# Optimization experiments

Measured on AMD Instinct MI355X. Metric: run time of the kernel, lower is better.

The kernel has to match this reference:

```python
import jax, jax.numpy as jnp
import numpy as np

B, T, C = 2, 1536, 1536
H, K, V = 8, 64, 192
NPF = 192            # num_position_features
NB = NPF // 6        # basis per class for central_mask, asymmetric (6 components)
FD = 2 * NB          # actual positional feature dim after sign concat
R = 2 * T - 1


def central_mask_feats(positions, num_basis, seq_length):
    # widths grow geometrically so only |pos| < width activates (central mask)
    pow_rate = np.exp(np.log(seq_length + 1) / num_basis).astype(np.float32)
    widths = jnp.power(pow_rate, jnp.arange(1, num_basis + 1, dtype=jnp.float32)) - 1.0
    return (widths[None, :] > jnp.abs(positions)[:, None]).astype(jnp.float32)


def position_features(positions, seq_length):
    emb = central_mask_feats(positions, NB, seq_length)                 # [R, NB]
    return jnp.concatenate([emb, jnp.sign(positions)[:, None] * emb], axis=-1)  # [R, 2*NB]


def relative_shift(x):
    # x: [B, H, T, 2T-1] -> [B, H, T, T] (Transformer-XL shift trick)
    b, h, t, r = x.shape
    x = jnp.pad(x, ((0, 0), (0, 0), (0, 0), (1, 0)))    # [B,H,T,2T]
    x = x.reshape(b, h, 2 * t, t)[:, :, 1:, :]          # [B,H,2T-1,T]
    x = x.reshape(b, h, t, 2 * t - 1)[..., :t]          # [B,H,T,T]
    return x


def setup_inputs() -> dict:
    key = jax.random.key(0)
    ks = jax.random.split(key, 9)
    s = 0.02
    return {
        "x": jax.random.normal(ks[0], (B, T, C), jnp.float32),
        "Wq": jax.random.normal(ks[1], (C, H * K), jnp.float32) * s,
        "Wk": jax.random.normal(ks[2], (C, H * K), jnp.float32) * s,
        "Wv": jax.random.normal(ks[3], (C, H * V), jnp.float32) * s,
        "Wrk": jax.random.normal(ks[4], (FD, H * K), jnp.float32) * s,
        "r_w_bias": jax.random.normal(ks[5], (1, H, 1, K), jnp.float32) * s,
        "r_r_bias": jax.random.normal(ks[6], (1, H, 1, K), jnp.float32) * s,
        "Wo": jax.random.normal(ks[7], (H * V, H * V), jnp.float32) * s,
        "bo": jnp.zeros((H * V,), jnp.float32),
    }


def reference(x, Wq, Wk, Wv, Wrk, r_w_bias, r_r_bias, Wo, bo):
    b, t, _ = x.shape
    q = (x @ Wq).reshape(b, t, H, K).transpose(0, 2, 1, 3)   # [B,H,T,K]
    k = (x @ Wk).reshape(b, t, H, K).transpose(0, 2, 1, 3)
    v = (x @ Wv).reshape(b, t, H, V).transpose(0, 2, 1, 3)   # [B,H,T,V]
    q = q * (K ** -0.5)                                       # scaling=True

    # content logits with content bias r_w_bias
    content = jnp.einsum('bhqd,bhkd->bhqk', q + r_w_bias, k)  # [B,H,T,T]

    # relative position logits with position bias r_r_bias
    dists = jnp.arange(-(t - 1), t, dtype=jnp.float32)        # [2T-1]
    pos = position_features(dists, t)                         # [2T-1, FD]
    r_k = (pos @ Wrk).reshape(R, H, K).transpose(1, 0, 2)     # [H,2T-1,K]
    rel = jnp.einsum('bhqd,hrd->bhqr', q + r_r_bias, r_k)     # [B,H,T,2T-1]
    rel = relative_shift(rel)                                 # [B,H,T,T]

    logits = content + rel                                    # content_position_bias=True
    w = jax.nn.softmax(logits, axis=-1)
    out = jnp.einsum('bhqk,bhkv->bhqv', w, v)                 # [B,H,T,V]
    out = out.transpose(0, 2, 1, 3).reshape(b, t, H * V)      # [B,T,H*V]
    return out @ Wo + bo
```

## Files before the change

kernel.cpp:

```cpp
#include <hip/hip_runtime.h>
#include <hip/hip_bf16.h>
#include <math.h>

#define T_SEQ 1536
#define CDIM  1536
#define HEADS 8
#define DK    64
#define DV    192
#define HK    (HEADS * DK)
#define HV    (HEADS * DV)
#define RWIN  (2 * T_SEQ - 1)

typedef __attribute__((ext_vector_type(8))) short bf16x8;
typedef __attribute__((ext_vector_type(4))) float f32x4;

__device__ __forceinline__ unsigned short f2bf(float v) {
  __hip_bfloat16 h = __float2bfloat16(v);
  return *reinterpret_cast<unsigned short*>(&h);
}
__device__ __forceinline__ float bf2f(unsigned short u) {
  unsigned int x = ((unsigned int)u) << 16;
  union { unsigned int i; float f; } c; c.i = x; return c.f;
}

__global__ __launch_bounds__(256) void cast_bf16_kernel(
    const float* __restrict__ in, unsigned short* __restrict__ out, int n)
{
  const int i = (blockIdx.x * 256 + threadIdx.x) * 4;
  if (i >= n) return;
  const float4 v = *reinterpret_cast<const float4*>(&in[i]);
  ushort4 o;
  o.x = f2bf(v.x); o.y = f2bf(v.y); o.z = f2bf(v.z); o.w = f2bf(v.w);
  *reinterpret_cast<ushort4*>(&out[i]) = o;
}

__global__ __launch_bounds__(256) void tcast_kernel(
    const float* __restrict__ W, unsigned short* __restrict__ Wt, int Kd, int N)
{
  __shared__ float tile[32][33];
  const int n0 = blockIdx.x * 32, k0 = blockIdx.y * 32;
  const int tx = threadIdx.x, ty = threadIdx.y;
  #pragma unroll
  for (int i = 0; i < 32; i += 8)
    tile[ty + i][tx] = W[(size_t)(k0 + ty + i) * N + n0 + tx];
  __syncthreads();
  #pragma unroll
  for (int i = 0; i < 32; i += 8)
    Wt[(size_t)(n0 + ty + i) * Kd + k0 + tx] = f2bf(tile[tx][ty + i]);
}

template<int OMODE>
__global__ __launch_bounds__(256) void gemm_bf16_kernel(
    const unsigned short* __restrict__ A, const unsigned short* __restrict__ Bt,
    void* __restrict__ Cp, int M, int N, int Kd, float scale,
    const float* __restrict__ bias)
{
  constexpr int LDK = 40;
  __shared__ unsigned short As[128 * LDK];
  __shared__ unsigned short Bs[128 * LDK];
  const int tid = threadIdx.x;
  const int lane = tid & 63, wave = tid >> 6;
  const int wr = wave >> 1, wc = wave & 1;
  const int m0 = blockIdx.x * 128, n0 = blockIdx.y * 128;

  const int lr = tid >> 2;
  const int lc = (tid & 3) * 8;
  const int frow = lane & 15;
  const int fk = (lane >> 4) * 8;

  f32x4 acc[4][4];
  #pragma unroll
  for (int i = 0; i < 4; ++i)
    #pragma unroll
    for (int j = 0; j < 4; ++j) acc[i][j] = (f32x4){0.f, 0.f, 0.f, 0.f};

  uint4 a0 = *reinterpret_cast<const uint4*>(&A[(size_t)(m0 + lr) * Kd + lc]);
  uint4 a1 = *reinterpret_cast<const uint4*>(&A[(size_t)(m0 + 64 + lr) * Kd + lc]);
  uint4 b0 = *reinterpret_cast<const uint4*>(&Bt[(size_t)(n0 + lr) * Kd + lc]);
  uint4 b1 = *reinterpret_cast<const uint4*>(&Bt[(size_t)(n0 + 64 + lr) * Kd + lc]);

  for (int k0 = 0; k0 < Kd; k0 += 32) {
    __syncthreads();
    *reinterpret_cast<uint4*>(&As[lr * LDK + lc]) = a0;
    *reinterpret_cast<uint4*>(&As[(64 + lr) * LDK + lc]) = a1;
    *reinterpret_cast<uint4*>(&Bs[lr * LDK + lc]) = b0;
    *reinterpret_cast<uint4*>(&Bs[(64 + lr) * LDK + lc]) = b1;
    __syncthreads();
    if (k0 + 32 < Kd) {
      const int kn = k0 + 32;
      a0 = *reinterpret_cast<const uint4*>(&A[(size_t)(m0 + lr) * Kd + kn + lc]);
      a1 = *reinterpret_cast<const uint4*>(&A[(size_t)(m0 + 64 + lr) * Kd + kn + lc]);
      b0 = *reinterpret_cast<const uint4*>(&Bt[(size_t)(n0 + lr) * Kd + kn + lc]);
      b1 = *reinterpret_cast<const uint4*>(&Bt[(size_t)(n0 + 64 + lr) * Kd + kn + lc]);
    }
    bf16x8 af[4], bfr[4];
    #pragma unroll
    for (int mi = 0; mi < 4; ++mi)
      af[mi] = *reinterpret_cast<const bf16x8*>(&As[(wr * 64 + mi * 16 + frow) * LDK + fk]);
    #pragma unroll
    for (int ni = 0; ni < 4; ++ni)
      bfr[ni] = *reinterpret_cast<const bf16x8*>(&Bs[(wc * 64 + ni * 16 + frow) * LDK + fk]);
    #pragma unroll
    for (int mi = 0; mi < 4; ++mi)
      #pragma unroll
      for (int ni = 0; ni < 4; ++ni)
        acc[mi][ni] = __builtin_amdgcn_mfma_f32_16x16x32_bf16(af[mi], bfr[ni], acc[mi][ni], 0, 0, 0);
  }

  const int er = (lane >> 4) * 4;
  #pragma unroll
  for (int mi = 0; mi < 4; ++mi)
    #pragma unroll
    for (int ni = 0; ni < 4; ++ni) {
      const int n = n0 + wc * 64 + ni * 16 + frow;
      if constexpr (OMODE == 2) {
        const int mrow0 = m0 + wr * 64 + mi * 16 + er;
        const int bb = mrow0 / T_SEQ;
        const int t0 = mrow0 - bb * T_SEQ;
        ushort4 pk;
        pk.x = f2bf(acc[mi][ni][0] * scale);
        pk.y = f2bf(acc[mi][ni][1] * scale);
        pk.z = f2bf(acc[mi][ni][2] * scale);
        pk.w = f2bf(acc[mi][ni][3] * scale);
        *reinterpret_cast<ushort4*>(
            &((unsigned short*)Cp)[((size_t)bb * HV + n) * T_SEQ + t0]) = pk;
      } else {
        #pragma unroll
        for (int r = 0; r < 4; ++r) {
          const int m = m0 + wr * 64 + mi * 16 + er + r;
          float v = acc[mi][ni][r] * scale;
          if constexpr (OMODE == 0) {
            if (bias != nullptr) v += bias[n];
            ((float*)Cp)[(size_t)m * N + n] = v;
          } else {
            ((unsigned short*)Cp)[(size_t)m * N + n] = f2bf(v);
          }
        }
      }
    }
}

__global__ __launch_bounds__(512) void rk_kernel(
    const float* __restrict__ Wrk, unsigned short* __restrict__ rk)
{
  const int r = blockIdx.x;
  const int t = threadIdx.x;
  __shared__ float pos[64];

  if (t < 64) {
    const double d = (double)(r - (T_SEQ - 1));
    const int j = t & 31;
    const double pr = exp(log((double)(T_SEQ + 1)) / 32.0);
    const double w = pow(pr, (double)(j + 1)) - 1.0;
    const float emb = (w > fabs(d)) ? 1.0f : 0.0f;
    const float sgn = (d > 0.0) ? 1.f : ((d < 0.0) ? -1.f : 0.f);
    pos[t] = (t < 32) ? emb : sgn * emb;
  }
  __syncthreads();

  float acc = 0.f;
  #pragma unroll 8
  for (int f = 0; f < 64; ++f) acc = fmaf(pos[f], Wrk[f * HK + t], acc);

  const int h = t >> 6, kk = t & 63;
  rk[((size_t)h * RWIN + r) * DK + kk] = f2bf(acc);
}

__global__ __launch_bounds__(256, 2) void attn_mfma_kernel(
    const float* __restrict__ qf, const unsigned short* __restrict__ kb,
    const unsigned short* __restrict__ vt, const unsigned short* __restrict__ rkb,
    const float* __restrict__ rwb, const float* __restrict__ rrb,
    unsigned short* __restrict__ ab)
{
  const int it = blockIdx.x, h = blockIdx.y, b = blockIdx.z;
  const int i0 = it * 64;
  const int tid = threadIdx.x, lane = tid & 63, wv = tid >> 6;
  const int cl = lane & 15, g4 = 4 * (lane >> 4), kb8 = 8 * (lane >> 4);

  __shared__ unsigned short Klds[64][72];
  __shared__ unsigned short Vlds[192][72];
  __shared__ unsigned short Rbuf[64][132];
  __shared__ unsigned short Plds[64][72];

  bf16x8 qwf[2], qrf[2];
  {
    const int qrow = b * T_SEQ + i0 + 16 * wv + cl;
    const float* qp = &qf[(size_t)qrow * HK + h * DK];
    #pragma unroll
    for (int kf = 0; kf < 2; ++kf) {
      bf16x8 tw, tr;
      #pragma unroll
      for (int e = 0; e < 8; ++e) {
        const int k = kb8 + 32 * kf + e;
        const float qv = qp[k];
        tw[e] = (short)f2bf(qv + rwb[h * DK + k]);
        tr[e] = (short)f2bf(qv + rrb[h * DK + k]);
      }
      qwf[kf] = tw; qrf[kf] = tr;
    }
  }

  uint4 kreg[2], vreg[6];
  auto load_tiles = [&](int j0) {
    #pragma unroll
    for (int c = 0; c < 2; ++c) {
      const int idx = tid + 256 * c;
      kreg[c] = *reinterpret_cast<const uint4*>(
          &kb[((size_t)(b * T_SEQ + j0 + (idx >> 3))) * HK + h * DK + (idx & 7) * 8]);
    }
    #pragma unroll
    for (int c = 0; c < 6; ++c) {
      const int idx = tid + 256 * c;
      vreg[c] = *reinterpret_cast<const uint4*>(
          &vt[((size_t)b * HV + h * DV + (idx >> 3)) * T_SEQ + j0 + (idx & 7) * 8]);
    }
  };
  auto store_tiles = [&]() {
    #pragma unroll
    for (int c = 0; c < 2; ++c) {
      const int idx = tid + 256 * c;
      *reinterpret_cast<uint4*>(&Klds[idx >> 3][(idx & 7) * 8]) = kreg[c];
    }
    #pragma unroll
    for (int c = 0; c < 6; ++c) {
      const int idx = tid + 256 * c;
      *reinterpret_cast<uint4*>(&Vlds[idx >> 3][(idx & 7) * 8]) = vreg[c];
    }
  };

  auto computeR = [&](int base) {
    #pragma unroll
    for (int f = 0; f < 4; ++f) {
      f32x4 rr = (f32x4){0.f, 0.f, 0.f, 0.f};
      #pragma unroll
      for (int ks = 0; ks < 2; ++ks) {
        int row = base + 16 * f + cl;
        row = row < 0 ? 0 : row;
        const bf16x8 bfrag = *reinterpret_cast<const bf16x8*>(
            &rkb[((size_t)h * RWIN + row) * DK + kb8 + 32 * ks]);
        rr = __builtin_amdgcn_mfma_f32_16x16x32_bf16(qrf[ks], bfrag, rr, 0, 0, 0);
      }
      const int irow = 16 * wv + g4;
      const int slot = (base + 16 * f + cl) & 127;
      #pragma unroll
      for (int r = 0; r < 4; ++r)
        Rbuf[irow + r][slot] = f2bf(rr[r]);
    }
  };

  float mrun[4] = {-1e30f, -1e30f, -1e30f, -1e30f};
  float lrun[4] = {0.f, 0.f, 0.f, 0.f};
  f32x4 o[12];
  #pragma unroll
  for (int vf = 0; vf < 12; ++vf) o[vf] = (f32x4){0.f, 0.f, 0.f, 0.f};

  const int D0 = T_SEQ - 1 - i0;
  load_tiles(0);
  computeR(D0 - 64);
  int Dj = D0;

  for (int jt = 0; jt < T_SEQ / 64; ++jt) {
    __syncthreads();
    store_tiles();
    __syncthreads();
    if (jt + 1 < T_SEQ / 64) load_tiles((jt + 1) * 64);

    computeR(Dj);

    f32x4 s[4];
    #pragma unroll
    for (int f = 0; f < 4; ++f) {
      s[f] = (f32x4){0.f, 0.f, 0.f, 0.f};
      #pragma unroll
      for (int ks = 0; ks < 2; ++ks) {
        const bf16x8 kfrag = *reinterpret_cast<const bf16x8*>(
            &Klds[16 * f + cl][kb8 + 32 * ks]);
        s[f] = __builtin_amdgcn_mfma_f32_16x16x32_bf16(qwf[ks], kfrag, s[f], 0, 0, 0);
      }
    }
    #pragma unroll
    for (int f = 0; f < 4; ++f)
      #pragma unroll
      for (int r = 0; r < 4; ++r) {
        const int iloc = 16 * wv + g4 + r;
        const int slot = (Dj + 16 * f + cl - iloc) & 127;
        s[f][r] += bf2f(Rbuf[iloc][slot]);
      }
    #pragma unroll
    for (int r = 0; r < 4; ++r) {
      float mx = fmaxf(fmaxf(s[0][r], s[1][r]), fmaxf(s[2][r], s[3][r]));
      mx = fmaxf(mx, __shfl_xor(mx, 1));
      mx = fmaxf(mx, __shfl_xor(mx, 2));
      mx = fmaxf(mx, __shfl_xor(mx, 4));
      mx = fmaxf(mx, __shfl_xor(mx, 8));
      const float mnew = fmaxf(mrun[r], mx);
      const float fac = __expf(mrun[r] - mnew);
      mrun[r] = mnew;
      float ps = 0.f;
      #pragma unroll
      for (int f = 0; f < 4; ++f) {
        const float p = __expf(s[f][r] - mnew);
        ps += p;
        Plds[16 * wv + g4 + r][16 * f + cl] = f2bf(p);
      }
      ps += __shfl_xor(ps, 1);
      ps += __shfl_xor(ps, 2);
      ps += __shfl_xor(ps, 4);
      ps += __shfl_xor(ps, 8);
      lrun[r] = lrun[r] * fac + ps;
      #pragma unroll
      for (int vf = 0; vf < 12; ++vf) o[vf][r] *= fac;
    }
    #pragma unroll
    for (int ks = 0; ks < 2; ++ks) {
      const bf16x8 pfrag = *reinterpret_cast<const bf16x8*>(
          &Plds[16 * wv + cl][kb8 + 32 * ks]);
      #pragma unroll
      for (int vf = 0; vf < 12; ++vf) {
        const bf16x8 vfrag = *reinterpret_cast<const bf16x8*>(
            &Vlds[16 * vf + cl][kb8 + 32 * ks]);
        o[vf] = __builtin_amdgcn_mfma_f32_16x16x32_bf16(pfrag, vfrag, o[vf], 0, 0, 0);
      }
    }
    Dj += 64;
  }

  #pragma unroll
  for (int r = 0; r < 4; ++r) {
    const float inv = 1.f / lrun[r];
    const size_t gi = (size_t)(b * T_SEQ + i0 + 16 * wv + g4 + r);
    #pragma unroll
    for (int vf = 0; vf < 12; ++vf) {
      const int v = 16 * vf + cl;
      ab[gi * HV + h * DV + v] = f2bf(o[vf][r] * inv);
    }
  }
}

extern "C" void kernel_launch(void* const* d_in, const int* in_sizes, int n_in,
                              void* d_out, int out_size, void* d_ws, size_t ws_size,
                              hipStream_t stream) {
  const float* x   = (const float*)d_in[0];
  const float* Wq  = (const float*)d_in[1];
  const float* Wk  = (const float*)d_in[2];
  const float* Wv  = (const float*)d_in[3];
  const float* Wrk = (const float*)d_in[4];
  const float* rwb = (const float*)d_in[5];
  const float* rrb = (const float*)d_in[6];
  const float* Wo  = (const float*)d_in[7];
  const float* bo  = (const float*)d_in[8];
  float* out = (float*)d_out;

  const int BT = 2 * T_SEQ;

  char* w = (char*)d_ws;
  float* qf           = (float*)w;          w += (size_t)BT * HK * 4;
  unsigned short* kbuf = (unsigned short*)w; w += (size_t)BT * HK * 2;
  unsigned short* vtb  = (unsigned short*)w; w += (size_t)2 * HV * T_SEQ * 2;
  unsigned short* rkb  = (unsigned short*)w; w += (size_t)HEADS * RWIN * DK * 2;
  unsigned short* xb   = (unsigned short*)w; w += (size_t)BT * CDIM * 2;
  unsigned short* ab   = (unsigned short*)w; w += (size_t)BT * HV * 2;
  unsigned short* Wqt  = (unsigned short*)w; w += (size_t)HK * CDIM * 2;
  unsigned short* Wkt  = (unsigned short*)w; w += (size_t)HK * CDIM * 2;
  unsigned short* Wvt  = (unsigned short*)w; w += (size_t)HV * CDIM * 2;
  unsigned short* Wot  = (unsigned short*)w; w += (size_t)HV * CDIM * 2;

  const int nx = BT * CDIM;

  cast_bf16_kernel<<<nx / 1024, 256, 0, stream>>>(x, xb, nx);
  tcast_kernel<<<dim3(HK / 32, CDIM / 32), dim3(32, 8), 0, stream>>>(Wq, Wqt, CDIM, HK);
  tcast_kernel<<<dim3(HK / 32, CDIM / 32), dim3(32, 8), 0, stream>>>(Wk, Wkt, CDIM, HK);
  tcast_kernel<<<dim3(HV / 32, CDIM / 32), dim3(32, 8), 0, stream>>>(Wv, Wvt, CDIM, HV);
  tcast_kernel<<<dim3(HV / 32, CDIM / 32), dim3(32, 8), 0, stream>>>(Wo, Wot, CDIM, HV);

  gemm_bf16_kernel<0><<<dim3(BT / 128, HK / 128), 256, 0, stream>>>(
      xb, Wqt, qf, BT, HK, CDIM, 0.125f, nullptr);
  gemm_bf16_kernel<1><<<dim3(BT / 128, HK / 128), 256, 0, stream>>>(
      xb, Wkt, kbuf, BT, HK, CDIM, 1.0f, nullptr);
  gemm_bf16_kernel<2><<<dim3(BT / 128, HV / 128), 256, 0, stream>>>(
      xb, Wvt, vtb, BT, HV, CDIM, 1.0f, nullptr);

  rk_kernel<<<RWIN, 512, 0, stream>>>(Wrk, rkb);

  attn_mfma_kernel<<<dim3(T_SEQ / 64, HEADS, 2), 256, 0, stream>>>(
      qf, kbuf, vtb, rkb, rwb, rrb, ab);

  gemm_bf16_kernel<0><<<dim3(BT / 128, HV / 128), 256, 0, stream>>>(
      ab, Wot, out, BT, HV, CDIM, 1.0f, bo);
}
```

Baseline: 417.3 us.

## Read K/V fragments directly from global memory in attention, drop LDS staging

The attention kernel stops staging K and V tiles through shared memory with block barriers and instead loads MFMA fragments straight from global memory (relying on L2/L1). LDS use drops, so occupancy is raised to 4 blocks per CU, and blocks are remapped so each XCD handles contiguous (b,h) work for cache locality. The V GEMM now writes row-major output and a separate transpose kernel builds V^T, and the output buffer aliases the x bf16 buffer. s_setprio is raised around the PV MFMA loop. Risks: uncoalesced, higher-latency global fragment reads and an extra transpose pass.

```diff
diff --git a/kernel.cpp b/kernel.cpp
--- a/kernel.cpp
+++ b/kernel.cpp
@@ -47,6 +47,21 @@
   #pragma unroll
   for (int i = 0; i < 32; i += 8)
     Wt[(size_t)(n0 + ty + i) * Kd + k0 + tx] = f2bf(tile[tx][ty + i]);
+}
+
+__global__ __launch_bounds__(256) void vtrans_kernel(
+    const unsigned short* __restrict__ in, unsigned short* __restrict__ out)
+{
+  __shared__ unsigned short tile[32][33];
+  const int v0 = blockIdx.x * 32, t0 = blockIdx.y * 32, b = blockIdx.z;
+  const int tx = threadIdx.x, ty = threadIdx.y;
+  #pragma unroll
+  for (int i = 0; i < 32; i += 8)
+    tile[ty + i][tx] = in[(size_t)(b * T_SEQ + t0 + ty + i) * HV + v0 + tx];
+  __syncthreads();
+  #pragma unroll
+  for (int i = 0; i < 32; i += 8)
+    out[((size_t)b * HV + v0 + ty + i) * T_SEQ + t0 + tx] = tile[tx][ty + i];
 }
 
 template<int OMODE>
@@ -113,28 +128,15 @@
     #pragma unroll
     for (int ni = 0; ni < 4; ++ni) {
       const int n = n0 + wc * 64 + ni * 16 + frow;
-      if constexpr (OMODE == 2) {
-        const int mrow0 = m0 + wr * 64 + mi * 16 + er;
-        const int bb = mrow0 / T_SEQ;
-        const int t0 = mrow0 - bb * T_SEQ;
-        ushort4 pk;
-        pk.x = f2bf(acc[mi][ni][0] * scale);
-        pk.y = f2bf(acc[mi][ni][1] * scale);
-        pk.z = f2bf(acc[mi][ni][2] * scale);
-        pk.w = f2bf(acc[mi][ni][3] * scale);
-        *reinterpret_cast<ushort4*>(
-            &((unsigned short*)Cp)[((size_t)bb * HV + n) * T_SEQ + t0]) = pk;
-      } else {
-        #pragma unroll
-        for (int r = 0; r < 4; ++r) {
-          const int m = m0 + wr * 64 + mi * 16 + er + r;
-          float v = acc[mi][ni][r] * scale;
-          if constexpr (OMODE == 0) {
-            if (bias != nullptr) v += bias[n];
-            ((float*)Cp)[(size_t)m * N + n] = v;
-          } else {
-            ((unsigned short*)Cp)[(size_t)m * N + n] = f2bf(v);
-          }
+      #pragma unroll
+      for (int r = 0; r < 4; ++r) {
+        const int m = m0 + wr * 64 + mi * 16 + er + r;
+        float v = acc[mi][ni][r] * scale;
+        if constexpr (OMODE == 0) {
+          if (bias != nullptr) v += bias[n];
+          ((float*)Cp)[(size_t)m * N + n] = v;
+        } else {
+          ((unsigned short*)Cp)[(size_t)m * N + n] = f2bf(v);
         }
       }
     }
@@ -166,19 +168,21 @@
   rk[((size_t)h * RWIN + r) * DK + kk] = f2bf(acc);
 }
 
-__global__ __launch_bounds__(256, 2) void attn_mfma_kernel(
+__global__ __launch_bounds__(256, 4) void attn_mfma_kernel(
     const float* __restrict__ qf, const unsigned short* __restrict__ kb,
     const unsigned short* __restrict__ vt, const unsigned short* __restrict__ rkb,
     const float* __restrict__ rwb, const float* __restrict__ rrb,
     unsigned short* __restrict__ ab)
 {
-  const int it = blockIdx.x, h = blockIdx.y, b = blockIdx.z;
+  const int bid = blockIdx.x;
+  const int wk = (bid & 7) * 48 + (bid >> 3);
+  const int it = wk % 24;
+  const int h  = (wk / 24) & 7;
+  const int b  = wk / 192;
   const int i0 = it * 64;
   const int tid = threadIdx.x, lane = tid & 63, wv = tid >> 6;
   const int cl = lane & 15, g4 = 4 * (lane >> 4), kb8 = 8 * (lane >> 4);
 
-  __shared__ unsigned short Klds[64][72];
-  __shared__ unsigned short Vlds[192][72];
   __shared__ unsigned short Rbuf[64][132];
   __shared__ unsigned short Plds[64][72];
 
@@ -199,34 +203,6 @@
       qwf[kf] = tw; qrf[kf] = tr;
     }
   }
-
-  uint4 kreg[2], vreg[6];
-  auto load_tiles = [&](int j0) {
-    #pragma unroll
-    for (int c = 0; c < 2; ++c) {
-      const int idx = tid + 256 * c;
-      kreg[c] = *reinterpret_cast<const uint4*>(
-          &kb[((size_t)(b * T_SEQ + j0 + (idx >> 3))) * HK + h * DK + (idx & 7) * 8]);
-    }
-    #pragma unroll
-    for (int c = 0; c < 6; ++c) {
-      const int idx = tid + 256 * c;
-      vreg[c] = *reinterpret_cast<const uint4*>(
-          &vt[((size_t)b * HV + h * DV + (idx >> 3)) * T_SEQ + j0 + (idx & 7) * 8]);
-    }
-  };
-  auto store_tiles = [&]() {
-    #pragma unroll
-    for (int c = 0; c < 2; ++c) {
-      const int idx = tid + 256 * c;
-      *reinterpret_cast<uint4*>(&Klds[idx >> 3][(idx & 7) * 8]) = kreg[c];
-    }
-    #pragma unroll
-    for (int c = 0; c < 6; ++c) {
-      const int idx = tid + 256 * c;
-      *reinterpret_cast<uint4*>(&Vlds[idx >> 3][(idx & 7) * 8]) = vreg[c];
-    }
-  };
 
   auto computeR = [&](int base) {
     #pragma unroll
@@ -255,16 +231,14 @@
   for (int vf = 0; vf < 12; ++vf) o[vf] = (f32x4){0.f, 0.f, 0.f, 0.f};
 
   const int D0 = T_SEQ - 1 - i0;
-  load_tiles(0);
   computeR(D0 - 64);
   int Dj = D0;
 
+  const unsigned short* kbase = &kb[(size_t)(b * T_SEQ) * HK + h * DK];
+  const unsigned short* vbase = &vt[((size_t)b * HV + h * DV) * T_SEQ];
+
   for (int jt = 0; jt < T_SEQ / 64; ++jt) {
-    __syncthreads();
-    store_tiles();
-    __syncthreads();
-    if (jt + 1 < T_SEQ / 64) load_tiles((jt + 1) * 64);
-
+    const int j0 = jt * 64;
     computeR(Dj);
 
     f32x4 s[4];
@@ -274,7 +248,7 @@
       #pragma unroll
       for (int ks = 0; ks < 2; ++ks) {
         const bf16x8 kfrag = *reinterpret_cast<const bf16x8*>(
-            &Klds[16 * f + cl][kb8 + 32 * ks]);
+            &kbase[(size_t)(j0 + 16 * f + cl) * HK + kb8 + 32 * ks]);
         s[f] = __builtin_amdgcn_mfma_f32_16x16x32_bf16(qwf[ks], kfrag, s[f], 0, 0, 0);
       }
     }
@@ -311,6 +285,7 @@
       #pragma unroll
       for (int vf = 0; vf < 12; ++vf) o[vf][r] *= fac;
     }
+    __builtin_amdgcn_s_setprio(1);
     #pragma unroll
     for (int ks = 0; ks < 2; ++ks) {
       const bf16x8 pfrag = *reinterpret_cast<const bf16x8*>(
@@ -318,10 +293,11 @@
       #pragma unroll
       for (int vf = 0; vf < 12; ++vf) {
         const bf16x8 vfrag = *reinterpret_cast<const bf16x8*>(
-            &Vlds[16 * vf + cl][kb8 + 32 * ks]);
+            &vbase[(size_t)(16 * vf + cl) * T_SEQ + j0 + kb8 + 32 * ks]);
         o[vf] = __builtin_amdgcn_mfma_f32_16x16x32_bf16(pfrag, vfrag, o[vf], 0, 0, 0);
       }
     }
+    __builtin_amdgcn_s_setprio(0);
     Dj += 64;
   }
 
@@ -354,16 +330,17 @@
   const int BT = 2 * T_SEQ;
 
   char* w = (char*)d_ws;
-  float* qf           = (float*)w;          w += (size_t)BT * HK * 4;
+  float* qf            = (float*)w;          w += (size_t)BT * HK * 4;
   unsigned short* kbuf = (unsigned short*)w; w += (size_t)BT * HK * 2;
+  unsigned short* vb   = (unsigned short*)w; w += (size_t)BT * HV * 2;
   unsigned short* vtb  = (unsigned short*)w; w += (size_t)2 * HV * T_SEQ * 2;
   unsigned short* rkb  = (unsigned short*)w; w += (size_t)HEADS * RWIN * DK * 2;
   unsigned short* xb   = (unsigned short*)w; w += (size_t)BT * CDIM * 2;
-  unsigned short* ab   = (unsigned short*)w; w += (size_t)BT * HV * 2;
   unsigned short* Wqt  = (unsigned short*)w; w += (size_t)HK * CDIM * 2;
   unsigned short* Wkt  = (unsigned short*)w; w += (size_t)HK * CDIM * 2;
   unsigned short* Wvt  = (unsigned short*)w; w += (size_t)HV * CDIM * 2;
   unsigned short* Wot  = (unsigned short*)w; w += (size_t)HV * CDIM * 2;
+  unsigned short* ab   = xb;
 
   const int nx = BT * CDIM;
 
@@ -377,12 +354,14 @@
       xb, Wqt, qf, BT, HK, CDIM, 0.125f, nullptr);
   gemm_bf16_kernel<1><<<dim3(BT / 128, HK / 128), 256, 0, stream>>>(
       xb, Wkt, kbuf, BT, HK, CDIM, 1.0f, nullptr);
-  gemm_bf16_kernel<2><<<dim3(BT / 128, HV / 128), 256, 0, stream>>>(
-      xb, Wvt, vtb, BT, HV, CDIM, 1.0f, nullptr);
+  gemm_bf16_kernel<1><<<dim3(BT / 128, HV / 128), 256, 0, stream>>>(
+      xb, Wvt, vb, BT, HV, CDIM, 1.0f, nullptr);
+
+  vtrans_kernel<<<dim3(HV / 32, T_SEQ / 32, 2), dim3(32, 8), 0, stream>>>(vb, vtb);
 
   rk_kernel<<<RWIN, 512, 0, stream>>>(Wrk, rkb);
 
-  attn_mfma_kernel<<<dim3(T_SEQ / 64, HEADS, 2), 256, 0, stream>>>(
+  attn_mfma_kernel<<<384, 256, 0, stream>>>(
       qf, kbuf, vtb, rkb, rwb, rrb, ab);
 
   gemm_bf16_kernel<0><<<dim3(BT / 128, HV / 128), 256, 0, stream>>>(
```

After: 519.4 us. +24.5%, slower.
